# Optimization experiments

Hardware: AMD Instinct MI355X
Metric: run time of the kernel (lower is better)

## Reference

```python
import jax, jax.numpy as jnp
import numpy as np

VOCAB = 50257
EMBED = 256
UNITS = 1024   # dec_units == attention units == GRU units
ENC_D = 1024   # encoder feature dim
B = 64
T_ENC = 128


def setup_inputs() -> dict:
    key = jax.random.key(0)
    ks = jax.random.split(key, 16)
    s = lambda k, *sh: jax.random.normal(k, sh, dtype=jnp.float32) * 0.02
    gru_in = ENC_D + EMBED  # concat(context, embedding)
    return {
        "x": jax.random.randint(ks[0], (B, 1), 0, VOCAB),
        "hidden": jax.random.normal(ks[1], (B, UNITS), dtype=jnp.float32),
        "enc_output": jax.random.normal(ks[2], (B, T_ENC, ENC_D), dtype=jnp.float32),
        "emb": s(ks[3], VOCAB, EMBED),
        "W1": s(ks[4], UNITS, UNITS), "b1": jnp.zeros((UNITS,), jnp.float32),
        "W2": s(ks[5], ENC_D, UNITS), "b2": jnp.zeros((UNITS,), jnp.float32),
        "V": s(ks[6], UNITS, 1), "bV": jnp.zeros((1,), jnp.float32),
        "gru_kernel": s(ks[7], gru_in, 3 * UNITS),
        "gru_rkernel": s(ks[8], UNITS, 3 * UNITS),
        "gru_bias": jnp.zeros((2, 3 * UNITS), jnp.float32),  # reset_after=True: [input_bias, recurrent_bias]
        "fcW": s(ks[9], UNITS, VOCAB), "fcb": jnp.zeros((VOCAB,), jnp.float32),
    }


def reference(x, hidden, enc_output, emb, W1, b1, W2, b2, V, bV,
              gru_kernel, gru_rkernel, gru_bias, fcW, fcb):
    # --- Bahdanau attention ---
    q = hidden[:, None, :] @ W1 + b1                    # [B,1,U]
    k = enc_output @ W2 + b2                            # [B,T,U]
    score = jnp.tanh(q + k) @ V + bV                    # [B,T,1]
    attw = jax.nn.softmax(score, axis=1)                # [B,T,1]
    context = jnp.sum(attw * enc_output, axis=1)        # [B,ENC_D]

    # --- embed token and concat (single time step) ---
    e = emb[x[:, 0]]                                    # [B,EMBED]
    xin = jnp.concatenate([context, e], axis=-1)        # [B,ENC_D+EMBED]

    # --- single GRU step (keras default reset_after=True), initial state zeros
    # (original code calls self.gru(x) without initial_state) ---
    h0 = jnp.zeros((xin.shape[0], UNITS), xin.dtype)
    xz, xr, xh = jnp.split(xin @ gru_kernel + gru_bias[0], 3, axis=-1)
    rz, rr, rh = jnp.split(h0 @ gru_rkernel + gru_bias[1], 3, axis=-1)
    z = jax.nn.sigmoid(xz + rz)
    r = jax.nn.sigmoid(xr + rr)
    hh = jnp.tanh(xh + r * rh)
    h = z * h0 + (1.0 - z) * hh                          # [B,U]

    logits = h @ fcW + fcb                               # [B,VOCAB]
    return logits, h, attw
```

## Files before the change

kernel.cpp:

```cpp
#include <hip/hip_runtime.h>
#include <hip/hip_bf16.h>

#define UNITS 1024
#define EMBED 256
#define TENC  128
#define BATCH 64
#define VOCAB 50257
#define GRU_IN 1280
#define MROWS 8192
#define NCB   8
#define NSPLIT 8

typedef __bf16 bf16x8 __attribute__((ext_vector_type(8)));
typedef float  f32x4  __attribute__((ext_vector_type(4)));
typedef float  f32x4u __attribute__((ext_vector_type(4), aligned(4)));

__device__ __forceinline__ void gload_lds16(const void* gsrc, void* ldst) {
  __builtin_amdgcn_global_load_lds(
      (const __attribute__((address_space(1))) void*)gsrc,
      (__attribute__((address_space(3))) void*)ldst,
      16, 0, 0);
}

__global__ __launch_bounds__(256) void prep_kernel(
    const float* __restrict__ enc, const float* __restrict__ W2,
    const float* __restrict__ hidden, const float* __restrict__ W1,
    __bf16* __restrict__ encb, __bf16* __restrict__ w2t,
    float* __restrict__ qpart)
{
  __shared__ __bf16 tl[64][72];
  __shared__ __bf16 As[2][4][64][8];
  __shared__ __bf16 Bs[2][4][64][8];
  const int bid = blockIdx.x;
  const int tid = threadIdx.x;

  if (bid < 4096) {
    const size_t base = ((size_t)bid * 256 + tid) * 8;
    const f32x4 v0 = *reinterpret_cast<const f32x4*>(enc + base);
    const f32x4 v1 = *reinterpret_cast<const f32x4*>(enc + base + 4);
    bf16x8 o;
#pragma unroll
    for (int j = 0; j < 4; ++j) { o[j] = (__bf16)v0[j]; o[4 + j] = (__bf16)v1[j]; }
    *reinterpret_cast<bf16x8*>(encb + base) = o;
    return;
  }
  if (bid < 4352) {
    const int ti  = bid - 4096;
    const int kt0 = (ti >> 4) * 64, nt0 = (ti & 15) * 64;
    const int r = tid >> 2, q = (tid & 3) * 16;
    const float* wp = W2 + (size_t)(kt0 + r) * UNITS + nt0 + q;
#pragma unroll
    for (int v = 0; v < 4; ++v) {
      const f32x4 a = *reinterpret_cast<const f32x4*>(wp + v * 4);
#pragma unroll
      for (int j = 0; j < 4; ++j) tl[r][q + v * 4 + j] = (__bf16)a[j];
    }
    __syncthreads();
    const int n = tid >> 2, kq = (tid & 3) * 16;
    bf16x8 o0, o1;
#pragma unroll
    for (int j = 0; j < 8; ++j) { o0[j] = tl[kq + j][n]; o1[j] = tl[kq + 8 + j][n]; }
    __bf16* op = w2t + (size_t)(nt0 + n) * UNITS + kt0 + kq;
    *reinterpret_cast<bf16x8*>(op)     = o0;
    *reinterpret_cast<bf16x8*>(op + 8) = o1;
    return;
  }

  const int idx   = bid - 4352;
  const int col0  = (idx & 15) * 64;
  const int kbase = (idx >> 4) * 128;
  const int lane = tid & 63;
  const int wid  = tid >> 6;
  const int wm   = (wid >> 1) * 32;
  const int wn   = (wid & 1) * 32;

  f32x4 acc[2][2] = {};
  const int ar  = tid >> 2;
  const int akc = (tid & 3) * 8;
  const int bkk = tid >> 4;
  const int bn  = (tid & 15) * 4;

  f32x4 pa0[2], pa1[2], pb0[2], pb1[2];
  auto LOAD = [&](int k0, int s) {
    const float* ap = hidden + (size_t)ar * UNITS + k0 + akc;
    pa0[s] = *reinterpret_cast<const f32x4*>(ap);
    pa1[s] = *reinterpret_cast<const f32x4*>(ap + 4);
    const float* bp0 = W1 + (size_t)(k0 + bkk) * UNITS + col0 + bn;
    pb0[s] = *reinterpret_cast<const f32x4*>(bp0);
    pb1[s] = *reinterpret_cast<const f32x4*>(bp0 + (size_t)16 * UNITS);
  };
  auto STAGE = [&](int s, int bb) {
    bf16x8 v;
#pragma unroll
    for (int j = 0; j < 4; ++j) { v[j] = (__bf16)pa0[s][j]; v[4 + j] = (__bf16)pa1[s][j]; }
    *reinterpret_cast<bf16x8*>(&As[bb][tid & 3][ar][0]) = v;
#pragma unroll
    for (int j = 0; j < 4; ++j) {
      Bs[bb][bkk >> 3][bn + j][bkk & 7]               = (__bf16)pb0[s][j];
      Bs[bb][(bkk + 16) >> 3][bn + j][(bkk + 16) & 7] = (__bf16)pb1[s][j];
    }
  };
  auto COMPUTE = [&](int bb) {
    bf16x8 af[2], bfr[2];
#pragma unroll
    for (int f = 0; f < 2; ++f) {
      af[f]  = *reinterpret_cast<const bf16x8*>(&As[bb][lane >> 4][wm + f * 16 + (lane & 15)][0]);
      bfr[f] = *reinterpret_cast<const bf16x8*>(&Bs[bb][lane >> 4][wn + f * 16 + (lane & 15)][0]);
    }
#pragma unroll
    for (int fm = 0; fm < 2; ++fm)
#pragma unroll
      for (int fn = 0; fn < 2; ++fn)
        acc[fm][fn] = __builtin_amdgcn_mfma_f32_16x16x32_bf16(af[fm], bfr[fn], acc[fm][fn], 0, 0, 0);
  };

  LOAD(kbase, 0);
  LOAD(kbase + 32, 1);
  STAGE(0, 0);
  __syncthreads();
#pragma unroll 1
  for (int t = 0; t < 4; t += 2) {
    if (t + 2 < 4) LOAD(kbase + ((t + 2) << 5), 0);
    COMPUTE(0);
    STAGE(1, 1);
    __syncthreads();
    if (t + 3 < 4) LOAD(kbase + ((t + 3) << 5), 1);
    COMPUTE(1);
    if (t + 2 < 4) STAGE(0, 0);
    __syncthreads();
  }

  float* Cz = qpart + (size_t)(idx >> 4) * BATCH * UNITS;
#pragma unroll
  for (int fm = 0; fm < 2; ++fm) {
    const int rbase = wm + fm * 16 + (lane >> 4) * 4;
#pragma unroll
    for (int fn = 0; fn < 2; ++fn) {
      const int gc = col0 + wn + fn * 16 + (lane & 15);
#pragma unroll
      for (int r = 0; r < 4; ++r)
        Cz[(size_t)(rbase + r) * UNITS + gc] = acc[fm][fn][r];
    }
  }
}

__global__ __launch_bounds__(256) void gemm_splitk(
    const float* __restrict__ A, const float* __restrict__ B,
    float* __restrict__ Cpart, int M, int N, int K, int Kc)
{
  const int col0  = blockIdx.y * 64;
  const int kbase = blockIdx.z * Kc;
  const int tid  = threadIdx.x;
  const int lane = tid & 63;
  const int wid  = tid >> 6;
  const int wm   = (wid >> 1) * 32;
  const int wn   = (wid & 1) * 32;

  __shared__ __bf16 As[2][4][64][8];
  __shared__ __bf16 Bs[2][4][64][8];

  f32x4 acc[2][2] = {};

  const int ar  = tid >> 2;
  const int akc = (tid & 3) * 8;
  const int bkk = tid >> 4;
  const int bn  = (tid & 15) * 4;

  f32x4 pa0[2], pa1[2], pb0[2], pb1[2];

  auto LOAD = [&](int k0, int s) {
    const float* ap = A + (size_t)ar * K + k0 + akc;
    pa0[s] = *reinterpret_cast<const f32x4*>(ap);
    pa1[s] = *reinterpret_cast<const f32x4*>(ap + 4);
    const float* bp0 = B + (size_t)(k0 + bkk) * N + col0 + bn;
    pb0[s] = *reinterpret_cast<const f32x4*>(bp0);
    pb1[s] = *reinterpret_cast<const f32x4*>(bp0 + (size_t)16 * N);
  };
  auto STAGE = [&](int s, int bb) {
    bf16x8 v;
#pragma unroll
    for (int j = 0; j < 4; ++j) { v[j] = (__bf16)pa0[s][j]; v[4 + j] = (__bf16)pa1[s][j]; }
    *reinterpret_cast<bf16x8*>(&As[bb][tid & 3][ar][0]) = v;
#pragma unroll
    for (int j = 0; j < 4; ++j) {
      Bs[bb][bkk >> 3][bn + j][bkk & 7]               = (__bf16)pb0[s][j];
      Bs[bb][(bkk + 16) >> 3][bn + j][(bkk + 16) & 7] = (__bf16)pb1[s][j];
    }
  };
  auto COMPUTE = [&](int bb) {
    bf16x8 af[2], bfr[2];
#pragma unroll
    for (int f = 0; f < 2; ++f) {
      af[f]  = *reinterpret_cast<const bf16x8*>(&As[bb][lane >> 4][wm + f * 16 + (lane & 15)][0]);
      bfr[f] = *reinterpret_cast<const bf16x8*>(&Bs[bb][lane >> 4][wn + f * 16 + (lane & 15)][0]);
    }
#pragma unroll
    for (int fm = 0; fm < 2; ++fm)
#pragma unroll
      for (int fn = 0; fn < 2; ++fn)
        acc[fm][fn] = __builtin_amdgcn_mfma_f32_16x16x32_bf16(af[fm], bfr[fn], acc[fm][fn], 0, 0, 0);
  };

  const int nt = Kc >> 5;
  LOAD(kbase, 0);
  LOAD(kbase + 32, 1);
  STAGE(0, 0);
  __syncthreads();
  for (int t = 0; t < nt; t += 2) {
    if (t + 2 < nt) LOAD(kbase + ((t + 2) << 5), 0);
    COMPUTE(0);
    if (t + 1 < nt) STAGE(1, 1);
    __syncthreads();
    if (t + 1 < nt) {
      if (t + 3 < nt) LOAD(kbase + ((t + 3) << 5), 1);
      COMPUTE(1);
      if (t + 2 < nt) STAGE(0, 0);
      __syncthreads();
    }
  }

  float* Cz = Cpart + (size_t)blockIdx.z * M * N;
#pragma unroll
  for (int fm = 0; fm < 2; ++fm) {
    const int rbase = wm + fm * 16 + (lane >> 4) * 4;
#pragma unroll
    for (int fn = 0; fn < 2; ++fn) {
      const int gc = col0 + wn + fn * 16 + (lane & 15);
#pragma unroll
      for (int r = 0; r < 4; ++r)
        Cz[(size_t)(rbase + r) * N + gc] = acc[fm][fn][r];
    }
  }
}

__global__ __launch_bounds__(256) void gemm_fc(
    const float* __restrict__ A, const float* __restrict__ B,
    const float* __restrict__ bias, float* __restrict__ C, int N)
{
  const int col0 = blockIdx.x * 64;
  const int tid  = threadIdx.x;
  const int lane = tid & 63;
  const int wid  = tid >> 6;
  const int wm   = (wid >> 1) * 32;
  const int wn   = (wid & 1) * 32;

  __shared__ __bf16 As[2][4][64][8];
  __shared__ __bf16 Bs[2][4][64][8];

  f32x4 acc[2][2] = {};

  const int ar  = tid >> 2;
  const int akc = (tid & 3) * 8;
  const int bkk = tid >> 4;
  const int bn  = (tid & 15) * 4;
  const int gn  = col0 + bn;
  const bool okb = (gn + 3 < N);

  f32x4 pa0[2], pa1[2], pb0[2], pb1[2];

  auto LOAD = [&](int k0, int s) {
    const float* ap = A + (size_t)ar * UNITS + k0 + akc;
    pa0[s] = *reinterpret_cast<const f32x4*>(ap);
    pa1[s] = *reinterpret_cast<const f32x4*>(ap + 4);
    const float* bp0 = B + (size_t)(k0 + bkk) * N + gn;
    const float* bp1 = bp0 + (size_t)16 * N;
    if (okb) {
      pb0[s] = *reinterpret_cast<const f32x4u*>(bp0);
      pb1[s] = *reinterpret_cast<const f32x4u*>(bp1);
    } else {
      f32x4 t0 = {0,0,0,0}, t1 = {0,0,0,0};
#pragma unroll
      for (int j = 0; j < 4; ++j)
        if (gn + j < N) { t0[j] = bp0[j]; t1[j] = bp1[j]; }
      pb0[s] = t0; pb1[s] = t1;
    }
  };
  auto STAGE = [&](int s, int bb) {
    bf16x8 v;
#pragma unroll
    for (int j = 0; j < 4; ++j) { v[j] = (__bf16)pa0[s][j]; v[4 + j] = (__bf16)pa1[s][j]; }
    *reinterpret_cast<bf16x8*>(&As[bb][tid & 3][ar][0]) = v;
#pragma unroll
    for (int j = 0; j < 4; ++j) {
      Bs[bb][bkk >> 3][bn + j][bkk & 7]               = (__bf16)pb0[s][j];
      Bs[bb][(bkk + 16) >> 3][bn + j][(bkk + 16) & 7] = (__bf16)pb1[s][j];
    }
  };
  auto COMPUTE = [&](int bb) {
    bf16x8 af[2], bfr[2];
#pragma unroll
    for (int f = 0; f < 2; ++f) {
      af[f]  = *reinterpret_cast<const bf16x8*>(&As[bb][lane >> 4][wm + f * 16 + (lane & 15)][0]);
      bfr[f] = *reinterpret_cast<const bf16x8*>(&Bs[bb][lane >> 4][wn + f * 16 + (lane & 15)][0]);
    }
#pragma unroll
    for (int fm = 0; fm < 2; ++fm)
#pragma unroll
      for (int fn = 0; fn < 2; ++fn)
        acc[fm][fn] = __builtin_amdgcn_mfma_f32_16x16x32_bf16(af[fm], bfr[fn], acc[fm][fn], 0, 0, 0);
  };

  LOAD(0, 0);
  LOAD(32, 1);
  STAGE(0, 0);
  __syncthreads();
#pragma unroll 1
  for (int t = 0; t < 32; t += 2) {
    if (t + 2 < 32) LOAD((t + 2) << 5, 0);
    COMPUTE(0);
    STAGE(1, 1);
    __syncthreads();
    if (t + 3 < 32) LOAD((t + 3) << 5, 1);
    COMPUTE(1);
    if (t + 2 < 32) STAGE(0, 0);
    __syncthreads();
  }

#pragma unroll
  for (int fm = 0; fm < 2; ++fm) {
    const int rbase = wm + fm * 16 + (lane >> 4) * 4;
#pragma unroll
    for (int fn = 0; fn < 2; ++fn) {
      const int gc = col0 + wn + fn * 16 + (lane & 15);
      if (gc >= N) continue;
      const float bv = bias[gc];
#pragma unroll
      for (int r = 0; r < 4; ++r)
        __builtin_nontemporal_store(acc[fm][fn][r] + bv, &C[(size_t)(rbase + r) * N + gc]);
    }
  }
}

__global__ __launch_bounds__(256) void k_score_mfma(
    const __bf16* __restrict__ encb, const __bf16* __restrict__ w2t,
    const float* __restrict__ b1, const float* __restrict__ b2,
    const float* __restrict__ qpart, const float* __restrict__ Vw,
    float* __restrict__ partial)
{
  const int b    = blockIdx.x;
  const int row0 = b * TENC;
  const int col0 = blockIdx.y * 128;
  const int tid  = threadIdx.x;
  const int lane = tid & 63;
  const int wid  = tid >> 6;
  const int wm   = (wid >> 1) * 64;
  const int wn   = (wid & 1) * 64;

  __shared__ __bf16 As[8][128][8];
  __shared__ __bf16 Bs[8][128][8];
  __shared__ float  sred[2][128];

  f32x4 acc[4][4] = {};

  for (int t = 0; t < 16; ++t) {
    const int k0 = t * 64;
#pragma unroll
    for (int j = 0; j < 4; ++j) {
      const int i  = wid * 4 + j;
      const int c  = i >> 1, rh = (i & 1) * 64;
      gload_lds16(encb + (size_t)(row0 + rh + lane) * UNITS + k0 + c * 8, &As[c][rh][0]);
      gload_lds16(w2t  + (size_t)(col0 + rh + lane) * UNITS + k0 + c * 8, &Bs[c][rh][0]);
    }
    __syncthreads();

#pragma unroll
    for (int s = 0; s < 2; ++s) {
      bf16x8 af[4], bfr[4];
#pragma unroll
      for (int f = 0; f < 4; ++f) {
        af[f]  = *reinterpret_cast<const bf16x8*>(&As[s * 4 + (lane >> 4)][wm + f * 16 + (lane & 15)][0]);
        bfr[f] = *reinterpret_cast<const bf16x8*>(&Bs[s * 4 + (lane >> 4)][wn + f * 16 + (lane & 15)][0]);
      }
#pragma unroll
      for (int fm = 0; fm < 4; ++fm)
#pragma unroll
        for (int fn = 0; fn < 4; ++fn)
          acc[fm][fn] = __builtin_amdgcn_mfma_f32_16x16x32_bf16(af[fm], bfr[fn], acc[fm][fn], 0, 0, 0);
    }
    __syncthreads();
  }

  float rowsum[4][4] = {};
#pragma unroll
  for (int fn = 0; fn < 4; ++fn) {
    const int gc = col0 + wn + fn * 16 + (lane & 15);
    float qv = b1[gc] + b2[gc];
#pragma unroll
    for (int s = 0; s < NSPLIT; ++s)
      qv += qpart[(size_t)s * BATCH * UNITS + (size_t)b * UNITS + gc];
    const float vv = Vw[gc];
#pragma unroll
    for (int fm = 0; fm < 4; ++fm)
#pragma unroll
      for (int r = 0; r < 4; ++r)
        rowsum[fm][r] += tanhf(qv + acc[fm][fn][r]) * vv;
  }
#pragma unroll
  for (int off = 8; off; off >>= 1)
#pragma unroll
    for (int fm = 0; fm < 4; ++fm)
#pragma unroll
      for (int r = 0; r < 4; ++r)
        rowsum[fm][r] += __shfl_xor(rowsum[fm][r], off);
  if ((lane & 15) == 0) {
#pragma unroll
    for (int fm = 0; fm < 4; ++fm)
#pragma unroll
      for (int r = 0; r < 4; ++r)
        sred[wid & 1][wm + fm * 16 + (lane >> 4) * 4 + r] = rowsum[fm][r];
  }
  __syncthreads();
  if (tid < TENC)
    partial[(size_t)blockIdx.y * MROWS + row0 + tid] = sred[0][tid] + sred[1][tid];
}

__global__ __launch_bounds__(256) void ctx_kernel(
    const float* __restrict__ enc, const float* __restrict__ partial,
    const float* __restrict__ bV, const float* __restrict__ emb,
    const int* __restrict__ x, float* __restrict__ attw,
    float* __restrict__ xin)
{
  const int b   = blockIdx.x;
  const int yb  = blockIdx.y;
  const int tid = threadIdx.x;
  const int g   = tid >> 6;
  const int n   = tid & 63;
  __shared__ float scs[TENC];
  __shared__ float red[4];
  __shared__ float csum[4][64];

  if (tid < TENC) {
    float s = bV[0];
#pragma unroll
    for (int cb = 0; cb < NCB; ++cb) s += partial[(size_t)cb * MROWS + b * TENC + tid];
    float m = s;
#pragma unroll
    for (int off = 32; off; off >>= 1) m = fmaxf(m, __shfl_xor(m, off));
    if ((tid & 63) == 0) red[tid >> 6] = m;
    scs[tid] = s;
  }
  __syncthreads();
  const float mm = fmaxf(red[0], red[1]);
  if (tid < TENC) {
    const float e = expf(scs[tid] - mm);
    scs[tid] = e;
    float su = e;
#pragma unroll
    for (int off = 32; off; off >>= 1) su += __shfl_xor(su, off);
    if ((tid & 63) == 0) red[2 + (tid >> 6)] = su;
  }
  __syncthreads();
  const float inv = 1.f / (red[2] + red[3]);

  if (yb == 0 && tid < TENC) attw[(size_t)b * TENC + tid] = scs[tid] * inv;

  const int n0 = yb * 64;
  const float* ep = enc + ((size_t)b * TENC + g * 32) * UNITS + n0 + n;
  float c = 0.f;
#pragma unroll 8
  for (int i = 0; i < 32; ++i) c += scs[g * 32 + i] * ep[(size_t)i * UNITS];
  csum[g][n] = c;
  __syncthreads();
  if (tid < 64)
    xin[(size_t)b * GRU_IN + n0 + tid] =
        (csum[0][tid] + csum[1][tid] + csum[2][tid] + csum[3][tid]) * inv;
  if (yb == 0)
    xin[(size_t)b * GRU_IN + UNITS + tid] = emb[(size_t)x[b] * EMBED + tid];
}

__global__ __launch_bounds__(256) void gru_pw(
    const float* __restrict__ gpart, const float* __restrict__ gb0,
    const float* __restrict__ gb1, float* __restrict__ h)
{
  const int i = blockIdx.x * 256 + threadIdx.x;
  const int b = i >> 10, n = i & 1023;
  float xz = gb0[n], xr = gb0[1024 + n], xh = gb0[2048 + n];
#pragma unroll
  for (int s = 0; s < NSPLIT; ++s) {
    const float* g = gpart + (size_t)s * BATCH * 3072 + (size_t)b * 3072;
    xz += g[n]; xr += g[1024 + n]; xh += g[2048 + n];
  }
  const float rz = gb1[n], rr = gb1[1024 + n], rh = gb1[2048 + n];
  const float z = 1.f / (1.f + expf(-(xz + rz)));
  const float r = 1.f / (1.f + expf(-(xr + rr)));
  const float hh = tanhf(xh + r * rh);
  h[i] = (1.f - z) * hh;
}

extern "C" void kernel_launch(void* const* d_in, const int* in_sizes, int n_in,
                              void* d_out, int out_size, void* d_ws, size_t ws_size,
                              hipStream_t stream)
{
  (void)in_sizes; (void)n_in; (void)out_size; (void)ws_size;
  const int*   x      = (const int*)  d_in[0];
  const float* hidden = (const float*)d_in[1];
  const float* enc    = (const float*)d_in[2];
  const float* emb    = (const float*)d_in[3];
  const float* W1     = (const float*)d_in[4];
  const float* b1     = (const float*)d_in[5];
  const float* W2     = (const float*)d_in[6];
  const float* b2     = (const float*)d_in[7];
  const float* Vw     = (const float*)d_in[8];
  const float* bV     = (const float*)d_in[9];
  const float* gk     = (const float*)d_in[10];
  const float* gb     = (const float*)d_in[12];
  const float* fcW    = (const float*)d_in[13];
  const float* fcb    = (const float*)d_in[14];

  float* ws      = (float*)d_ws;
  float* qpart   = ws;
  float* partial = qpart + 524288;
  float* xin     = partial + 65536;
  float* gpart   = xin + 81920;
  __bf16* encb   = (__bf16*)(gpart + 1572864);
  __bf16* w2t    = encb + (size_t)MROWS * UNITS;

  float* out    = (float*)d_out;
  float* logits = out;
  float* hout   = out + (size_t)BATCH * VOCAB;
  float* attw   = hout + BATCH * UNITS;

  hipLaunchKernelGGL(prep_kernel, dim3(4096 + 256 + 128), dim3(256), 0, stream,
                     enc, W2, hidden, W1, encb, w2t, qpart);
  hipLaunchKernelGGL(k_score_mfma, dim3(64, NCB), dim3(256), 0, stream,
                     encb, w2t, b1, b2, qpart, Vw, partial);
  hipLaunchKernelGGL(ctx_kernel, dim3(64, 16), dim3(256), 0, stream,
                     enc, partial, bV, emb, x, attw, xin);
  hipLaunchKernelGGL(gemm_splitk, dim3(1, 48, NSPLIT), dim3(256), 0, stream,
                     xin, gk, gpart, 64, 3072, 1280, 160);
  hipLaunchKernelGGL(gru_pw, dim3(256), dim3(256), 0, stream,
                     gpart, gb, gb + 3072, hout);
  hipLaunchKernelGGL(gemm_fc, dim3((VOCAB + 63) / 64), dim3(256), 0, stream,
                     hout, fcW, fcb, logits, VOCAB);
}
```

Baseline: 143.2 us.

## Fuse all decoder stages into one cooperative persistent kernel with grid syncs

Replaces the six-kernel launch sequence with a single cooperative mega_kernel of 512 persistent blocks. Each stage walks its work items in a grid-stride loop and is separated from the next by grid.sync, with the multi-kernel path kept as a fallback. The aim is to remove per-launch overhead and the gaps between kernels. In exchange every stage is capped at 512 blocks, so the vocab GEMM's 786 tiles and the 4480 prep items run in several waves, and each grid barrier has its own cost.

```diff
diff --git a/kernel.cpp b/kernel.cpp
--- a/kernel.cpp
+++ b/kernel.cpp
@@ -1,5 +1,8 @@
 #include <hip/hip_runtime.h>
 #include <hip/hip_bf16.h>
+#include <hip/hip_cooperative_groups.h>
+
+namespace cg = cooperative_groups;
 
 #define UNITS 1024
 #define EMBED 256
@@ -10,6 +13,7 @@
 #define MROWS 8192
 #define NCB   8
 #define NSPLIT 8
+#define NBLK  512
 
 typedef __bf16 bf16x8 __attribute__((ext_vector_type(8)));
 typedef float  f32x4  __attribute__((ext_vector_type(4)));
@@ -21,6 +25,7 @@
       (__attribute__((address_space(3))) void*)ldst,
       16, 0, 0);
 }
+
 
 __global__ __launch_bounds__(256) void prep_kernel(
     const float* __restrict__ enc, const float* __restrict__ W2,
@@ -114,21 +119,15 @@
         acc[fm][fn] = __builtin_amdgcn_mfma_f32_16x16x32_bf16(af[fm], bfr[fn], acc[fm][fn], 0, 0, 0);
   };
 
-  LOAD(kbase, 0);
-  LOAD(kbase + 32, 1);
-  STAGE(0, 0);
+  LOAD(kbase, 0); LOAD(kbase + 32, 1); STAGE(0, 0);
   __syncthreads();
-#pragma unroll 1
-  for (int t = 0; t < 4; t += 2) {
-    if (t + 2 < 4) LOAD(kbase + ((t + 2) << 5), 0);
-    COMPUTE(0);
-    STAGE(1, 1);
-    __syncthreads();
-    if (t + 3 < 4) LOAD(kbase + ((t + 3) << 5), 1);
-    COMPUTE(1);
-    if (t + 2 < 4) STAGE(0, 0);
-    __syncthreads();
-  }
+  LOAD(kbase + 64, 0); COMPUTE(0); STAGE(1, 1);
+  __syncthreads();
+  LOAD(kbase + 96, 1); COMPUTE(1); STAGE(0, 0);
+  __syncthreads();
+  COMPUTE(0); STAGE(1, 1);
+  __syncthreads();
+  COMPUTE(1);
 
   float* Cz = qpart + (size_t)(idx >> 4) * BATCH * UNITS;
 #pragma unroll
@@ -160,14 +159,12 @@
   __shared__ __bf16 Bs[2][4][64][8];
 
   f32x4 acc[2][2] = {};
-
   const int ar  = tid >> 2;
   const int akc = (tid & 3) * 8;
   const int bkk = tid >> 4;
   const int bn  = (tid & 15) * 4;
 
   f32x4 pa0[2], pa1[2], pb0[2], pb1[2];
-
   auto LOAD = [&](int k0, int s) {
     const float* ap = A + (size_t)ar * K + k0 + akc;
     pa0[s] = *reinterpret_cast<const f32x4*>(ap);
@@ -202,9 +199,7 @@
   };
 
   const int nt = Kc >> 5;
-  LOAD(kbase, 0);
-  LOAD(kbase + 32, 1);
-  STAGE(0, 0);
+  LOAD(kbase, 0); LOAD(kbase + 32, 1); STAGE(0, 0);
   __syncthreads();
   for (int t = 0; t < nt; t += 2) {
     if (t + 2 < nt) LOAD(kbase + ((t + 2) << 5), 0);
@@ -248,7 +243,6 @@
   __shared__ __bf16 Bs[2][4][64][8];
 
   f32x4 acc[2][2] = {};
-
   const int ar  = tid >> 2;
   const int akc = (tid & 3) * 8;
   const int bkk = tid >> 4;
@@ -257,7 +251,6 @@
   const bool okb = (gn + 3 < N);
 
   f32x4 pa0[2], pa1[2], pb0[2], pb1[2];
-
   auto LOAD = [&](int k0, int s) {
     const float* ap = A + (size_t)ar * UNITS + k0 + akc;
     pa0[s] = *reinterpret_cast<const f32x4*>(ap);
@@ -300,9 +293,7 @@
         acc[fm][fn] = __builtin_amdgcn_mfma_f32_16x16x32_bf16(af[fm], bfr[fn], acc[fm][fn], 0, 0, 0);
   };
 
-  LOAD(0, 0);
-  LOAD(32, 1);
-  STAGE(0, 0);
+  LOAD(0, 0); LOAD(32, 1); STAGE(0, 0);
   __syncthreads();
 #pragma unroll 1
   for (int t = 0; t < 32; t += 2) {
@@ -362,7 +353,6 @@
       gload_lds16(w2t  + (size_t)(col0 + rh + lane) * UNITS + k0 + c * 8, &Bs[c][rh][0]);
     }
     __syncthreads();
-
 #pragma unroll
     for (int s = 0; s < 2; ++s) {
       bf16x8 af[4], bfr[4];
@@ -485,6 +475,427 @@
   const float r = 1.f / (1.f + expf(-(xr + rr)));
   const float hh = tanhf(xh + r * rh);
   h[i] = (1.f - z) * hh;
+}
+
+
+union SMem {
+  struct { __bf16 A[8][128][8]; __bf16 B[8][128][8]; float sred[2][128]; } ks;
+  struct { __bf16 A[2][4][64][8]; __bf16 B[2][4][64][8]; } gm;
+  struct { __bf16 tl[64][72]; } tr;
+  struct { float scs[TENC]; float red[4]; float csum[4][64]; } cx;
+};
+
+__global__ __launch_bounds__(256, 2) void mega_kernel(
+    const int* __restrict__ x, const float* __restrict__ hidden,
+    const float* __restrict__ enc, const float* __restrict__ emb,
+    const float* __restrict__ W1, const float* __restrict__ b1,
+    const float* __restrict__ W2, const float* __restrict__ b2,
+    const float* __restrict__ Vw, const float* __restrict__ bV,
+    const float* __restrict__ gk, const float* __restrict__ gb,
+    const float* __restrict__ fcW, const float* __restrict__ fcb,
+    __bf16* __restrict__ encb, __bf16* __restrict__ w2t,
+    float* __restrict__ qpart, float* __restrict__ partial,
+    float* __restrict__ xin, float* __restrict__ gpart,
+    float* __restrict__ logits, float* __restrict__ hout,
+    float* __restrict__ attw)
+{
+  __shared__ SMem sm;
+  cg::grid_group grid = cg::this_grid();
+  const int bid  = blockIdx.x;
+  const int tid  = threadIdx.x;
+  const int lane = tid & 63;
+  const int wid  = tid >> 6;
+  const int nblk = gridDim.x;
+
+  for (int item = bid; item < 4480; item += nblk) {
+    if (item < 4096) {
+      const size_t base = ((size_t)item * 256 + tid) * 8;
+      const f32x4 v0 = *reinterpret_cast<const f32x4*>(enc + base);
+      const f32x4 v1 = *reinterpret_cast<const f32x4*>(enc + base + 4);
+      bf16x8 o;
+#pragma unroll
+      for (int j = 0; j < 4; ++j) { o[j] = (__bf16)v0[j]; o[4 + j] = (__bf16)v1[j]; }
+      *reinterpret_cast<bf16x8*>(encb + base) = o;
+    } else if (item < 4352) {
+      __syncthreads();
+      const int ti  = item - 4096;
+      const int kt0 = (ti >> 4) * 64, nt0 = (ti & 15) * 64;
+      const int r = tid >> 2, q = (tid & 3) * 16;
+      const float* wp = W2 + (size_t)(kt0 + r) * UNITS + nt0 + q;
+#pragma unroll
+      for (int v = 0; v < 4; ++v) {
+        const f32x4 a = *reinterpret_cast<const f32x4*>(wp + v * 4);
+#pragma unroll
+        for (int j = 0; j < 4; ++j) sm.tr.tl[r][q + v * 4 + j] = (__bf16)a[j];
+      }
+      __syncthreads();
+      const int n = tid >> 2, kq = (tid & 3) * 16;
+      bf16x8 o0, o1;
+#pragma unroll
+      for (int j = 0; j < 8; ++j) { o0[j] = sm.tr.tl[kq + j][n]; o1[j] = sm.tr.tl[kq + 8 + j][n]; }
+      __bf16* op = w2t + (size_t)(nt0 + n) * UNITS + kt0 + kq;
+      *reinterpret_cast<bf16x8*>(op)     = o0;
+      *reinterpret_cast<bf16x8*>(op + 8) = o1;
+    } else {
+      __syncthreads();
+      const int idx   = item - 4352;
+      const int col0  = (idx & 15) * 64;
+      const int kbase = (idx >> 4) * 128;
+      const int wm = (wid >> 1) * 32, wn = (wid & 1) * 32;
+      f32x4 acc[2][2] = {};
+      const int ar  = tid >> 2;
+      const int akc = (tid & 3) * 8;
+      const int bkk = tid >> 4;
+      const int bn  = (tid & 15) * 4;
+      f32x4 pa0[2], pa1[2], pb0[2], pb1[2];
+      auto LOAD = [&](int k0, int s) {
+        const float* ap = hidden + (size_t)ar * UNITS + k0 + akc;
+        pa0[s] = *reinterpret_cast<const f32x4*>(ap);
+        pa1[s] = *reinterpret_cast<const f32x4*>(ap + 4);
+        const float* bp0 = W1 + (size_t)(k0 + bkk) * UNITS + col0 + bn;
+        pb0[s] = *reinterpret_cast<const f32x4*>(bp0);
+        pb1[s] = *reinterpret_cast<const f32x4*>(bp0 + (size_t)16 * UNITS);
+      };
+      auto STAGE = [&](int s, int bb) {
+        bf16x8 v;
+#pragma unroll
+        for (int j = 0; j < 4; ++j) { v[j] = (__bf16)pa0[s][j]; v[4 + j] = (__bf16)pa1[s][j]; }
+        *reinterpret_cast<bf16x8*>(&sm.gm.A[bb][tid & 3][ar][0]) = v;
+#pragma unroll
+        for (int j = 0; j < 4; ++j) {
+          sm.gm.B[bb][bkk >> 3][bn + j][bkk & 7]               = (__bf16)pb0[s][j];
+          sm.gm.B[bb][(bkk + 16) >> 3][bn + j][(bkk + 16) & 7] = (__bf16)pb1[s][j];
+        }
+      };
+      auto COMPUTE = [&](int bb) {
+        bf16x8 af[2], bfr[2];
+#pragma unroll
+        for (int f = 0; f < 2; ++f) {
+          af[f]  = *reinterpret_cast<const bf16x8*>(&sm.gm.A[bb][lane >> 4][wm + f * 16 + (lane & 15)][0]);
+          bfr[f] = *reinterpret_cast<const bf16x8*>(&sm.gm.B[bb][lane >> 4][wn + f * 16 + (lane & 15)][0]);
+        }
+#pragma unroll
+        for (int fm = 0; fm < 2; ++fm)
+#pragma unroll
+          for (int fn = 0; fn < 2; ++fn)
+            acc[fm][fn] = __builtin_amdgcn_mfma_f32_16x16x32_bf16(af[fm], bfr[fn], acc[fm][fn], 0, 0, 0);
+      };
+      LOAD(kbase, 0); LOAD(kbase + 32, 1); STAGE(0, 0);
+      __syncthreads();
+      LOAD(kbase + 64, 0); COMPUTE(0); STAGE(1, 1);
+      __syncthreads();
+      LOAD(kbase + 96, 1); COMPUTE(1); STAGE(0, 0);
+      __syncthreads();
+      COMPUTE(0); STAGE(1, 1);
+      __syncthreads();
+      COMPUTE(1);
+      float* Cz = qpart + (size_t)(idx >> 4) * BATCH * UNITS;
+#pragma unroll
+      for (int fm = 0; fm < 2; ++fm) {
+        const int rbase = wm + fm * 16 + (lane >> 4) * 4;
+#pragma unroll
+        for (int fn = 0; fn < 2; ++fn) {
+          const int gc = col0 + wn + fn * 16 + (lane & 15);
+#pragma unroll
+          for (int r = 0; r < 4; ++r)
+            Cz[(size_t)(rbase + r) * UNITS + gc] = acc[fm][fn][r];
+        }
+      }
+    }
+  }
+  __threadfence();
+  grid.sync();
+
+  for (int item = bid; item < 512; item += nblk) {
+    __syncthreads();
+    const int b    = item & 63;
+    const int cb   = item >> 6;
+    const int row0 = b * TENC;
+    const int col0 = cb * 128;
+    const int wm = (wid >> 1) * 64, wn = (wid & 1) * 64;
+    f32x4 acc[4][4] = {};
+
+    for (int t = 0; t < 16; ++t) {
+      const int k0 = t * 64;
+#pragma unroll
+      for (int j = 0; j < 4; ++j) {
+        const int i  = wid * 4 + j;
+        const int c  = i >> 1, rh = (i & 1) * 64;
+        gload_lds16(encb + (size_t)(row0 + rh + lane) * UNITS + k0 + c * 8, &sm.ks.A[c][rh][0]);
+        gload_lds16(w2t  + (size_t)(col0 + rh + lane) * UNITS + k0 + c * 8, &sm.ks.B[c][rh][0]);
+      }
+      __syncthreads();
+#pragma unroll
+      for (int s = 0; s < 2; ++s) {
+        bf16x8 af[4], bfr[4];
+#pragma unroll
+        for (int f = 0; f < 4; ++f) {
+          af[f]  = *reinterpret_cast<const bf16x8*>(&sm.ks.A[s * 4 + (lane >> 4)][wm + f * 16 + (lane & 15)][0]);
+          bfr[f] = *reinterpret_cast<const bf16x8*>(&sm.ks.B[s * 4 + (lane >> 4)][wn + f * 16 + (lane & 15)][0]);
+        }
+#pragma unroll
+        for (int fm = 0; fm < 4; ++fm)
+#pragma unroll
+          for (int fn = 0; fn < 4; ++fn)
+            acc[fm][fn] = __builtin_amdgcn_mfma_f32_16x16x32_bf16(af[fm], bfr[fn], acc[fm][fn], 0, 0, 0);
+      }
+      __syncthreads();
+    }
+
+    float rowsum[4][4] = {};
+#pragma unroll
+    for (int fn = 0; fn < 4; ++fn) {
+      const int gc = col0 + wn + fn * 16 + (lane & 15);
+      float qv = b1[gc] + b2[gc];
+#pragma unroll
+      for (int s = 0; s < NSPLIT; ++s)
+        qv += qpart[(size_t)s * BATCH * UNITS + (size_t)b * UNITS + gc];
+      const float vv = Vw[gc];
+#pragma unroll
+      for (int fm = 0; fm < 4; ++fm)
+#pragma unroll
+        for (int r = 0; r < 4; ++r)
+          rowsum[fm][r] += tanhf(qv + acc[fm][fn][r]) * vv;
+    }
+#pragma unroll
+    for (int off = 8; off; off >>= 1)
+#pragma unroll
+      for (int fm = 0; fm < 4; ++fm)
+#pragma unroll
+        for (int r = 0; r < 4; ++r)
+          rowsum[fm][r] += __shfl_xor(rowsum[fm][r], off);
+    if ((lane & 15) == 0) {
+#pragma unroll
+      for (int fm = 0; fm < 4; ++fm)
+#pragma unroll
+        for (int r = 0; r < 4; ++r)
+          sm.ks.sred[wid & 1][wm + fm * 16 + (lane >> 4) * 4 + r] = rowsum[fm][r];
+    }
+    __syncthreads();
+    if (tid < TENC)
+      partial[(size_t)cb * MROWS + row0 + tid] = sm.ks.sred[0][tid] + sm.ks.sred[1][tid];
+  }
+  __threadfence();
+  grid.sync();
+
+  for (int item = bid; item < 1024; item += nblk) {
+    __syncthreads();
+    const int b  = item & 63;
+    const int yb = item >> 6;
+    const int gq = tid >> 6;
+    const int n  = tid & 63;
+    if (tid < TENC) {
+      float s = bV[0];
+#pragma unroll
+      for (int cb = 0; cb < NCB; ++cb) s += partial[(size_t)cb * MROWS + b * TENC + tid];
+      float m = s;
+#pragma unroll
+      for (int off = 32; off; off >>= 1) m = fmaxf(m, __shfl_xor(m, off));
+      if ((tid & 63) == 0) sm.cx.red[tid >> 6] = m;
+      sm.cx.scs[tid] = s;
+    }
+    __syncthreads();
+    const float mm = fmaxf(sm.cx.red[0], sm.cx.red[1]);
+    if (tid < TENC) {
+      const float e = expf(sm.cx.scs[tid] - mm);
+      sm.cx.scs[tid] = e;
+      float su = e;
+#pragma unroll
+      for (int off = 32; off; off >>= 1) su += __shfl_xor(su, off);
+      if ((tid & 63) == 0) sm.cx.red[2 + (tid >> 6)] = su;
+    }
+    __syncthreads();
+    const float inv = 1.f / (sm.cx.red[2] + sm.cx.red[3]);
+    if (yb == 0 && tid < TENC) attw[(size_t)b * TENC + tid] = sm.cx.scs[tid] * inv;
+
+    const int n0 = yb * 64;
+    const float* ep = enc + ((size_t)b * TENC + gq * 32) * UNITS + n0 + n;
+    float c = 0.f;
+#pragma unroll 8
+    for (int i = 0; i < 32; ++i) c += sm.cx.scs[gq * 32 + i] * ep[(size_t)i * UNITS];
+    sm.cx.csum[gq][n] = c;
+    __syncthreads();
+    if (tid < 64)
+      xin[(size_t)b * GRU_IN + n0 + tid] =
+          (sm.cx.csum[0][tid] + sm.cx.csum[1][tid] + sm.cx.csum[2][tid] + sm.cx.csum[3][tid]) * inv;
+    if (yb == 0)
+      xin[(size_t)b * GRU_IN + UNITS + tid] = emb[(size_t)x[b] * EMBED + tid];
+  }
+  __threadfence();
+  grid.sync();
+
+  for (int item = bid; item < 384; item += nblk) {
+    __syncthreads();
+    const int y = item % 48, z = item / 48;
+    const int col0 = y * 64, kbase = z * 160;
+    const int wm = (wid >> 1) * 32, wn = (wid & 1) * 32;
+    f32x4 acc[2][2] = {};
+    const int ar  = tid >> 2;
+    const int akc = (tid & 3) * 8;
+    const int bkk = tid >> 4;
+    const int bn  = (tid & 15) * 4;
+    f32x4 pa0[2], pa1[2], pb0[2], pb1[2];
+    auto LOAD = [&](int k0, int s) {
+      const float* ap = xin + (size_t)ar * GRU_IN + k0 + akc;
+      pa0[s] = *reinterpret_cast<const f32x4*>(ap);
+      pa1[s] = *reinterpret_cast<const f32x4*>(ap + 4);
+      const float* bp0 = gk + (size_t)(k0 + bkk) * 3072 + col0 + bn;
+      pb0[s] = *reinterpret_cast<const f32x4*>(bp0);
+      pb1[s] = *reinterpret_cast<const f32x4*>(bp0 + (size_t)16 * 3072);
+    };
+    auto STAGE = [&](int s, int bb) {
+      bf16x8 v;
+#pragma unroll
+      for (int j = 0; j < 4; ++j) { v[j] = (__bf16)pa0[s][j]; v[4 + j] = (__bf16)pa1[s][j]; }
+      *reinterpret_cast<bf16x8*>(&sm.gm.A[bb][tid & 3][ar][0]) = v;
+#pragma unroll
+      for (int j = 0; j < 4; ++j) {
+        sm.gm.B[bb][bkk >> 3][bn + j][bkk & 7]               = (__bf16)pb0[s][j];
+        sm.gm.B[bb][(bkk + 16) >> 3][bn + j][(bkk + 16) & 7] = (__bf16)pb1[s][j];
+      }
+    };
+    auto COMPUTE = [&](int bb) {
+      bf16x8 af[2], bfr[2];
+#pragma unroll
+      for (int f = 0; f < 2; ++f) {
+        af[f]  = *reinterpret_cast<const bf16x8*>(&sm.gm.A[bb][lane >> 4][wm + f * 16 + (lane & 15)][0]);
+        bfr[f] = *reinterpret_cast<const bf16x8*>(&sm.gm.B[bb][lane >> 4][wn + f * 16 + (lane & 15)][0]);
+      }
+#pragma unroll
+      for (int fm = 0; fm < 2; ++fm)
+#pragma unroll
+        for (int fn = 0; fn < 2; ++fn)
+          acc[fm][fn] = __builtin_amdgcn_mfma_f32_16x16x32_bf16(af[fm], bfr[fn], acc[fm][fn], 0, 0, 0);
+    };
+    LOAD(kbase, 0); LOAD(kbase + 32, 1); STAGE(0, 0);
+    __syncthreads();
+    for (int t = 0; t < 5; t += 2) {
+      if (t + 2 < 5) LOAD(kbase + ((t + 2) << 5), 0);
+      COMPUTE(0);
+      if (t + 1 < 5) STAGE(1, 1);
+      __syncthreads();
+      if (t + 1 < 5) {
+        if (t + 3 < 5) LOAD(kbase + ((t + 3) << 5), 1);
+        COMPUTE(1);
+        if (t + 2 < 5) STAGE(0, 0);
+        __syncthreads();
+      }
+    }
+    float* Cz = gpart + (size_t)z * BATCH * 3072;
+#pragma unroll
+    for (int fm = 0; fm < 2; ++fm) {
+      const int rbase = wm + fm * 16 + (lane >> 4) * 4;
+#pragma unroll
+      for (int fn = 0; fn < 2; ++fn) {
+        const int gc = col0 + wn + fn * 16 + (lane & 15);
+#pragma unroll
+        for (int r = 0; r < 4; ++r)
+          Cz[(size_t)(rbase + r) * 3072 + gc] = acc[fm][fn][r];
+      }
+    }
+  }
+  __threadfence();
+  grid.sync();
+
+  for (int item = bid; item < 256; item += nblk) {
+    const int i = item * 256 + tid;
+    const int b = i >> 10, n = i & 1023;
+    float xz = gb[n], xr = gb[1024 + n], xh = gb[2048 + n];
+#pragma unroll
+    for (int s = 0; s < NSPLIT; ++s) {
+      const float* g = gpart + (size_t)s * BATCH * 3072 + (size_t)b * 3072;
+      xz += g[n]; xr += g[1024 + n]; xh += g[2048 + n];
+    }
+    const float* gb1p = gb + 3072;
+    const float rz = gb1p[n], rr = gb1p[1024 + n], rh = gb1p[2048 + n];
+    const float z = 1.f / (1.f + expf(-(xz + rz)));
+    const float r = 1.f / (1.f + expf(-(xr + rr)));
+    const float hh = tanhf(xh + r * rh);
+    hout[i] = (1.f - z) * hh;
+  }
+  __threadfence();
+  grid.sync();
+
+  for (int item = bid; item < (VOCAB + 63) / 64; item += nblk) {
+    __syncthreads();
+    const int col0 = item * 64;
+    const int wm = (wid >> 1) * 32, wn = (wid & 1) * 32;
+    f32x4 acc[2][2] = {};
+    const int ar  = tid >> 2;
+    const int akc = (tid & 3) * 8;
+    const int bkk = tid >> 4;
+    const int bn  = (tid & 15) * 4;
+    const int gn  = col0 + bn;
+    const bool okb = (gn + 3 < VOCAB);
+    f32x4 pa0[2], pa1[2], pb0[2], pb1[2];
+    auto LOAD = [&](int k0, int s) {
+      const float* ap = hout + (size_t)ar * UNITS + k0 + akc;
+      pa0[s] = *reinterpret_cast<const f32x4*>(ap);
+      pa1[s] = *reinterpret_cast<const f32x4*>(ap + 4);
+      const float* bp0 = fcW + (size_t)(k0 + bkk) * VOCAB + gn;
+      const float* bp1 = bp0 + (size_t)16 * VOCAB;
+      if (okb) {
+        pb0[s] = *reinterpret_cast<const f32x4u*>(bp0);
+        pb1[s] = *reinterpret_cast<const f32x4u*>(bp1);
+      } else {
+        f32x4 t0 = {0,0,0,0}, t1 = {0,0,0,0};
+#pragma unroll
+        for (int j = 0; j < 4; ++j)
+          if (gn + j < VOCAB) { t0[j] = bp0[j]; t1[j] = bp1[j]; }
+        pb0[s] = t0; pb1[s] = t1;
+      }
+    };
+    auto STAGE = [&](int s, int bb) {
+      bf16x8 v;
+#pragma unroll
+      for (int j = 0; j < 4; ++j) { v[j] = (__bf16)pa0[s][j]; v[4 + j] = (__bf16)pa1[s][j]; }
+      *reinterpret_cast<bf16x8*>(&sm.gm.A[bb][tid & 3][ar][0]) = v;
+#pragma unroll
+      for (int j = 0; j < 4; ++j) {
+        sm.gm.B[bb][bkk >> 3][bn + j][bkk & 7]               = (__bf16)pb0[s][j];
+        sm.gm.B[bb][(bkk + 16) >> 3][bn + j][(bkk + 16) & 7] = (__bf16)pb1[s][j];
+      }
+    };
+    auto COMPUTE = [&](int bb) {
+      bf16x8 af[2], bfr[2];
+#pragma unroll
+      for (int f = 0; f < 2; ++f) {
+        af[f]  = *reinterpret_cast<const bf16x8*>(&sm.gm.A[bb][lane >> 4][wm + f * 16 + (lane & 15)][0]);
+        bfr[f] = *reinterpret_cast<const bf16x8*>(&sm.gm.B[bb][lane >> 4][wn + f * 16 + (lane & 15)][0]);
+      }
+#pragma unroll
+      for (int fm = 0; fm < 2; ++fm)
+#pragma unroll
+        for (int fn = 0; fn < 2; ++fn)
+          acc[fm][fn] = __builtin_amdgcn_mfma_f32_16x16x32_bf16(af[fm], bfr[fn], acc[fm][fn], 0, 0, 0);
+    };
+    LOAD(0, 0); LOAD(32, 1); STAGE(0, 0);
+    __syncthreads();
+#pragma unroll 1
+    for (int t = 0; t < 32; t += 2) {
+      if (t + 2 < 32) LOAD((t + 2) << 5, 0);
+      COMPUTE(0);
+      STAGE(1, 1);
+      __syncthreads();
+      if (t + 3 < 32) LOAD((t + 3) << 5, 1);
+      COMPUTE(1);
+      if (t + 2 < 32) STAGE(0, 0);
+      __syncthreads();
+    }
+#pragma unroll
+    for (int fm = 0; fm < 2; ++fm) {
+      const int rbase = wm + fm * 16 + (lane >> 4) * 4;
+#pragma unroll
+      for (int fn = 0; fn < 2; ++fn) {
+        const int gc = col0 + wn + fn * 16 + (lane & 15);
+        if (gc >= VOCAB) continue;
+        const float bv = fcb[gc];
+#pragma unroll
+        for (int r = 0; r < 4; ++r)
+          __builtin_nontemporal_store(acc[fm][fn][r] + bv, &logits[(size_t)(rbase + r) * VOCAB + gc]);
+      }
+    }
+  }
 }
 
 extern "C" void kernel_launch(void* const* d_in, const int* in_sizes, int n_in,
@@ -520,6 +931,24 @@
   float* hout   = out + (size_t)BATCH * VOCAB;
   float* attw   = hout + BATCH * UNITS;
 
+  int maxPerCU = 0;
+  hipError_t qe = hipOccupancyMaxActiveBlocksPerMultiprocessor(
+      &maxPerCU, reinterpret_cast<const void*>(mega_kernel), 256, 0);
+  hipError_t le = hipErrorUnknown;
+  if (qe == hipSuccess && maxPerCU >= 2) {
+    void* args[] = {
+      (void*)&x, (void*)&hidden, (void*)&enc, (void*)&emb,
+      (void*)&W1, (void*)&b1, (void*)&W2, (void*)&b2,
+      (void*)&Vw, (void*)&bV, (void*)&gk, (void*)&gb,
+      (void*)&fcW, (void*)&fcb,
+      (void*)&encb, (void*)&w2t, (void*)&qpart, (void*)&partial,
+      (void*)&xin, (void*)&gpart, (void*)&logits, (void*)&hout, (void*)&attw
+    };
+    le = hipLaunchCooperativeKernel(reinterpret_cast<const void*>(mega_kernel),
+                                    dim3(NBLK), dim3(256), args, 0, stream);
+  }
+  if (le == hipSuccess) return;
+
   hipLaunchKernelGGL(prep_kernel, dim3(4096 + 256 + 128), dim3(256), 0, stream,
                      enc, W2, hidden, W1, encb, w2t, qpart);
   hipLaunchKernelGGL(k_score_mfma, dim3(64, NCB), dim3(256), 0, stream,
```

New measurement: 142.4 us. Within noise of the previous version (-0.5%).
